# Kernel optimization log

Hardware: AMD Instinct MI355X
Metric: run time of the kernel (lower is better)

Reference implementation:

```python
import jax, jax.numpy as jnp
import numpy as np

B, N, HD = 2, 2048, 2048
NH, KVH = 16, 4
D = HD // NH          # 128
R = NH // KVH         # 4 (kv_ratio)
KVD = KVH * D         # 512


def setup_inputs() -> dict:
    key = jax.random.key(0)
    ks = jax.random.split(key, 6)
    s = 0.02
    return {
        "tokens": jax.random.normal(ks[0], (B, N, HD), jnp.float32),
        "norm_w": jnp.ones((HD,), jnp.float32),
        "Wq": jax.random.normal(ks[1], (HD, HD), jnp.float32) * s,
        "bq": jnp.zeros((HD,), jnp.float32),
        "Wk": jax.random.normal(ks[2], (KVD, HD), jnp.float32) * s,
        "bk": jnp.zeros((KVD,), jnp.float32),
        "Wv": jax.random.normal(ks[3], (KVD, HD), jnp.float32) * s,
        "bv": jnp.zeros((KVD,), jnp.float32),
        "Wo": jax.random.normal(ks[4], (HD, HD), jnp.float32) * s,
        "bo": jnp.zeros((HD,), jnp.float32),
    }


def reference(tokens, norm_w, Wq, bq, Wk, bk, Wv, bv, Wo, bo):
    # RMSNorm (torch default eps=None -> finfo eps), learnable weight
    eps = jnp.finfo(tokens.dtype).eps
    x = tokens * jax.lax.rsqrt(jnp.mean(tokens * tokens, axis=-1, keepdims=True) + eps) * norm_w

    # projections -> [B, heads, N, D]
    q = (x @ Wq.T + bq).reshape(B, N, NH, D).transpose(0, 2, 1, 3)
    k = (x @ Wk.T + bk).reshape(B, N, KVH, D).transpose(0, 2, 1, 3)
    v = (x @ Wv.T + bv).reshape(B, N, KVH, D).transpose(0, 2, 1, 3)

    # GQA via tiling the kv block (matches torch.cat of copies: head h uses kv head h % KVH)
    k = jnp.tile(k, (1, R, 1, 1))
    v = jnp.tile(v, (1, R, 1, 1))

    # Faithful (inverted) mask: True where j <= i, and True positions are masked out.
    mask = jnp.arange(N)[None, :] <= jnp.arange(N)[:, None]  # [N, N]

    # No 1/sqrt(D) scaling in the original
    scores = jnp.einsum('bhid,bhjd->bhij', q, k)
    scores = jnp.where(mask[None, None, :, :], jnp.float32(-1e9), scores)
    attn = jax.nn.softmax(scores, axis=-1)

    a = jnp.einsum('bhij,bhjd->bhid', attn, v)       # [B, NH, N, D]
    a = a.transpose(0, 2, 1, 3).reshape(B, N, HD)    # [B, N, HD]
    return a @ Wo.T + bo
```

## Files before the change

kernel.cpp:

```cpp
#include <hip/hip_runtime.h>

#define BB   2
#define NN   2048
#define HDIM 2048
#define NHD  16
#define KVHD 4
#define DD   128
#define KVW  1024
#define MTOK (BB*NN)

typedef _Float16 h8 __attribute__((ext_vector_type(8)));
typedef _Float16 h4 __attribute__((ext_vector_type(4)));
typedef float    f4 __attribute__((ext_vector_type(4)));
typedef short    b8 __attribute__((ext_vector_type(8)));

static __device__ __forceinline__ f4 mfma16(h8 a, h8 b, f4 c) {
    return __builtin_amdgcn_mfma_f32_16x16x32_f16(a, b, c, 0, 0, 0);
}
static __device__ __forceinline__ f4 mfma16b(b8 a, b8 b, f4 c) {
    return __builtin_amdgcn_mfma_f32_16x16x32_bf16(a, b, c, 0, 0, 0);
}

static __device__ __forceinline__ unsigned short f2bf(float f) {
    unsigned int u = __float_as_uint(f);
    u += 0x7FFF + ((u >> 16) & 1);
    return (unsigned short)(u >> 16);
}

static __device__ __forceinline__ void gload_lds16(const void* g, void* l) {
    __builtin_amdgcn_global_load_lds(
        (const __attribute__((address_space(1))) void*)g,
        (__attribute__((address_space(3))) void*)l, 16, 0, 0);
}

__global__ __launch_bounds__(256) void rmsnorm_k(const float* __restrict__ t,
                                                 const float* __restrict__ wn,
                                                 _Float16* __restrict__ xh) {
    const int row = blockIdx.x, tid = threadIdx.x;
    const float* rp = t + (size_t)row * HDIM;
    float4 v[2];
    float ss = 0.f;
    #pragma unroll
    for (int p = 0; p < 2; ++p) {
        float4 x = *(const float4*)(rp + (p * 256 + tid) * 4);
        v[p] = x;
        ss += x.x * x.x + x.y * x.y + x.z * x.z + x.w * x.w;
    }
    #pragma unroll
    for (int off = 32; off; off >>= 1) ss += __shfl_xor(ss, off, 64);
    __shared__ float sred[4];
    if ((tid & 63) == 0) sred[tid >> 6] = ss;
    __syncthreads();
    float rs = rsqrtf((sred[0] + sred[1] + sred[2] + sred[3]) * (1.0f / HDIM)
                      + 1.1920928955078125e-07f);
    _Float16* op = xh + (size_t)row * HDIM;
    #pragma unroll
    for (int p = 0; p < 2; ++p) {
        int base = (p * 256 + tid) * 4;
        float4 w = *(const float4*)(wn + base);
        h4 o;
        o[0] = (_Float16)(v[p].x * rs * w.x);
        o[1] = (_Float16)(v[p].y * rs * w.y);
        o[2] = (_Float16)(v[p].z * rs * w.z);
        o[3] = (_Float16)(v[p].w * rs * w.w);
        *(h4*)(op + base) = o;
    }
}

__global__ __launch_bounds__(256) void cvt_k(const float* __restrict__ src,
                                             _Float16* __restrict__ dst, int n) {
    int i = (blockIdx.x * 256 + threadIdx.x) * 4;
    if (i < n) {
        float4 v = *(const float4*)(src + i);
        h4 o; o[0] = (_Float16)v.x; o[1] = (_Float16)v.y;
        o[2] = (_Float16)v.z; o[3] = (_Float16)v.w;
        *(h4*)(dst + i) = o;
    }
}

__global__ void biascat_k(const float* __restrict__ bk, const float* __restrict__ bv,
                          float* __restrict__ bkv, float* __restrict__ vsum) {
    int i = blockIdx.x * 256 + threadIdx.x;
    bkv[i] = (i < 512) ? bk[i] : bv[i - 512];
    vsum[i] = 0.f;
}

__global__ __launch_bounds__(256) void vtrans_k(const _Float16* __restrict__ kv,
                                                unsigned short* __restrict__ vt) {
    const int tid = threadIdx.x;
    const int tok = blockIdx.x * 64 + (tid & 63);
    const int kvh = blockIdx.y;
    const int d0 = (tid >> 6) * 32;
    const int b = tok >> 11, n = tok & (NN - 1);
    const _Float16* src = kv + (size_t)tok * KVW + 512 + kvh * DD + d0;
    unsigned short* dstb = vt + ((size_t)(b * KVHD + kvh) * DD) * NN + n;
    #pragma unroll
    for (int u = 0; u < 4; ++u) {
        h8 v = *(const h8*)(src + u * 8);
        #pragma unroll
        for (int e = 0; e < 8; ++e)
            dstb[(size_t)(d0 + u * 8 + e) * NN] = f2bf((float)v[e]);
    }
}

template <int OUTF32>
__global__ __launch_bounds__(256, 2) void gemm_bt(const _Float16* __restrict__ A,
                                                  const _Float16* __restrict__ Bw,
                                                  const float* __restrict__ bias,
                                                  void* __restrict__ Cout,
                                                  int Ndim, int K) {
    __shared__ _Float16 sA[128 * 64];
    __shared__ _Float16 sB[128 * 64];
    const int tid = threadIdx.x;
    const int lane = tid & 63, w = tid >> 6;
    const int ln = lane & 15, quad = lane >> 4;
    const int wm = w >> 1, wn = w & 1;
    const int m0 = blockIdx.y * 128, n0 = blockIdx.x * 128;

    f4 acc[4][4] = {};
    for (int k0 = 0; k0 < K; k0 += 64) {
        #pragma unroll
        for (int it = 0; it < 4; ++it) {
            int chunk = it * 256 + tid;
            int row = chunk >> 3, p = chunk & 7;
            int c = p ^ (row & 7);
            gload_lds16(A + (size_t)(m0 + row) * K + k0 + c * 8, sA + chunk * 8);
            gload_lds16(Bw + (size_t)(n0 + row) * K + k0 + c * 8, sB + chunk * 8);
        }
        __syncthreads();
        #pragma unroll
        for (int kk = 0; kk < 2; ++kk) {
            h8 af[4], bf[4];
            #pragma unroll
            for (int mt = 0; mt < 4; ++mt)
                af[mt] = *(const h8*)&sA[(wm * 64 + mt * 16 + ln) * 64 +
                                         (((kk * 4 + quad) ^ (ln & 7)) << 3)];
            #pragma unroll
            for (int nt = 0; nt < 4; ++nt)
                bf[nt] = *(const h8*)&sB[(wn * 64 + nt * 16 + ln) * 64 +
                                         (((kk * 4 + quad) ^ (ln & 7)) << 3)];
            #pragma unroll
            for (int mt = 0; mt < 4; ++mt)
                #pragma unroll
                for (int nt = 0; nt < 4; ++nt)
                    acc[mt][nt] = mfma16(af[mt], bf[nt], acc[mt][nt]);
        }
        __syncthreads();
    }
    #pragma unroll
    for (int mt = 0; mt < 4; ++mt) {
        int rowb = m0 + wm * 64 + mt * 16 + quad * 4;
        #pragma unroll
        for (int nt = 0; nt < 4; ++nt) {
            int col = n0 + wn * 64 + nt * 16 + ln;
            float bv = bias[col];
            #pragma unroll
            for (int r = 0; r < 4; ++r) {
                float v = acc[mt][nt][r] + bv;
                if (OUTF32)
                    ((float*)Cout)[(size_t)(rowb + r) * Ndim + col] = v;
                else
                    ((_Float16*)Cout)[(size_t)(rowb + r) * Ndim + col] = (_Float16)v;
            }
        }
    }
}

__global__ __launch_bounds__(512, 2) void attn_k(const _Float16* __restrict__ qh,
                                                 const _Float16* __restrict__ kvp,
                                                 const unsigned short* __restrict__ vt,
                                                 _Float16* __restrict__ ah) {
    __shared__ _Float16 s_k[2][32 * 128];
    __shared__ unsigned short s_v[2][128 * 32];
    __shared__ unsigned short s_p[8][32 * 32];
    const int tid = threadIdx.x;
    const int lane = tid & 63, w = tid >> 6;
    const int ln = lane & 15, quad = lane >> 4;
    const int wl = w & 3, half = w >> 2;
    const int u = blockIdx.x;
    const int h = blockIdx.y, b = blockIdx.z;
    const int it0 = half ? (15 - u) : u;
    const int i0 = it0 * 128;
    const int kvh = h & 3;
    const int my_begin = it0 * 4;

    h8 qf[2][4];
    #pragma unroll
    for (int t = 0; t < 2; ++t) {
        const _Float16* qrow =
            qh + ((size_t)(b * NN + i0 + wl * 32 + t * 16 + ln)) * HDIM + h * DD;
        #pragma unroll
        for (int kc = 0; kc < 4; ++kc)
            qf[t][kc] = *(const h8*)(qrow + kc * 32 + quad * 8);
    }

    b8 ones;
    #pragma unroll
    for (int e = 0; e < 8; ++e) ones[e] = (short)0x3F80;

    f4 O[2][8] = {};
    f4 OS[2] = {};

    auto stage = [&](int jt, int bufi) {
        const int j0 = jt * 32;
        {
            int jj = tid >> 4, p = tid & 15;
            int c = p ^ (jj & 15);
            gload_lds16(kvp + ((size_t)(b * NN + j0 + jj)) * KVW + kvh * DD + c * 8,
                        &s_k[bufi][tid * 8]);
        }
        {
            int d = tid >> 2, p = tid & 3;
            int c = p ^ ((d & 3) ^ ((d >> 2) & 3));
            gload_lds16(vt + ((size_t)(b * KVHD + kvh) * DD + d) * NN + j0 + c * 8,
                        &s_v[bufi][tid * 8]);
        }
    };

    const int blk_begin = u * 4;
    stage(blk_begin, 0);
    for (int jt = blk_begin; jt < NN / 32; ++jt) {
        const int j0 = jt * 32;
        const int cur = (jt - blk_begin) & 1;
        __syncthreads();
        if (jt + 1 < NN / 32) stage(jt + 1, cur ^ 1);

        if (jt >= my_begin) {
            f4 sc[2][2] = {};
            #pragma unroll
            for (int nt = 0; nt < 2; ++nt)
                #pragma unroll
                for (int kc = 0; kc < 4; ++kc) {
                    h8 bf = *(const h8*)&s_k[cur][(nt * 16 + ln) * 128 +
                                                  (((kc * 4 + quad) ^ ln) << 3)];
                    sc[0][nt] = mfma16(qf[0][kc], bf, sc[0][nt]);
                    sc[1][nt] = mfma16(qf[1][kc], bf, sc[1][nt]);
                }

            const bool need_mask = (jt < my_begin + 4);
            #pragma unroll
            for (int t = 0; t < 2; ++t) {
                #pragma unroll
                for (int r = 0; r < 4; ++r) {
                    int rr = t * 16 + quad * 4 + r;
                    int sw = r ^ quad;
                    #pragma unroll
                    for (int nt = 0; nt < 2; ++nt) {
                        float s = sc[t][nt][r];
                        if (need_mask) {
                            int ig = i0 + wl * 32 + t * 16 + quad * 4 + r;
                            int jg = j0 + nt * 16 + ln;
                            if (jg <= ig) s = -1e9f;
                        }
                        float p = __expf(s);
                        int c = nt * 2 + (ln >> 3);
                        s_p[w][rr * 32 + ((c ^ sw) << 3) + (ln & 7)] = f2bf(p);
                    }
                }
            }

            const int sv = (ln & 3) ^ ((ln >> 2) & 3);
            #pragma unroll
            for (int t = 0; t < 2; ++t) {
                b8 ap = *(const b8*)&s_p[w][(t * 16 + ln) * 32 + ((quad ^ sv) << 3)];
                #pragma unroll
                for (int dt = 0; dt < 8; ++dt) {
                    b8 bv = *(const b8*)&s_v[cur][(dt * 16 + ln) * 32 +
                                                  ((quad ^ sv) << 3)];
                    O[t][dt] = mfma16b(ap, bv, O[t][dt]);
                }
                OS[t] = mfma16b(ap, ones, OS[t]);
            }
        }
    }

    #pragma unroll
    for (int t = 0; t < 2; ++t) {
        float inv_l[4];
        #pragma unroll
        for (int r = 0; r < 4; ++r) inv_l[r] = 1.0f / OS[t][r];
        #pragma unroll
        for (int dt = 0; dt < 8; ++dt)
            #pragma unroll
            for (int r = 0; r < 4; ++r)
                ah[((size_t)(b * NN + i0 + wl * 32 + t * 16 + quad * 4 + r)) * HDIM +
                   h * DD + dt * 16 + ln] = (_Float16)(O[t][dt][r] * inv_l[r]);
    }
}

__global__ __launch_bounds__(256) void vsum_k(const _Float16* __restrict__ kvp,
                                              float* __restrict__ vsum) {
    __shared__ float red[16][128];
    const int seg = blockIdx.x, kvh = blockIdx.y, b = blockIdx.z;
    const int tid = threadIdx.x;
    const int jj = tid >> 4, dc = (tid & 15) * 8;
    float acc[8] = {};
    #pragma unroll 4
    for (int j = seg * 256 + jj; j < seg * 256 + 256; j += 16) {
        h8 v = *(const h8*)(kvp + ((size_t)(b * NN + j)) * KVW + 512 + kvh * DD + dc);
        #pragma unroll
        for (int e = 0; e < 8; ++e) acc[e] += (float)v[e];
    }
    #pragma unroll
    for (int e = 0; e < 8; ++e) red[jj][dc + e] = acc[e];
    __syncthreads();
    if (tid < 128) {
        float s = 0.f;
        #pragma unroll
        for (int t = 0; t < 16; ++t) s += red[t][tid];
        atomicAdd(&vsum[(b * KVHD + kvh) * DD + tid], s);
    }
}

__global__ void fixup_write_k(const float* __restrict__ vsum,
                              _Float16* __restrict__ ah) {
    int b = blockIdx.x >> 2, kvh = blockIdx.x & 3, d = threadIdx.x;
    float mean = vsum[(b * KVHD + kvh) * DD + d] * (1.0f / NN);
    #pragma unroll
    for (int r = 0; r < 4; ++r) {
        int h = r * 4 + kvh;
        ah[((size_t)(b * NN + NN - 1)) * HDIM + h * DD + d] = (_Float16)mean;
    }
}

extern "C" void kernel_launch(void* const* d_in, const int* in_sizes, int n_in,
                              void* d_out, int out_size, void* d_ws, size_t ws_size,
                              hipStream_t stream) {
    const float* tokens = (const float*)d_in[0];
    const float* norm_w = (const float*)d_in[1];
    const float* Wq = (const float*)d_in[2];
    const float* bq = (const float*)d_in[3];
    const float* Wk = (const float*)d_in[4];
    const float* bk = (const float*)d_in[5];
    const float* Wv = (const float*)d_in[6];
    const float* bv = (const float*)d_in[7];
    const float* Wo = (const float*)d_in[8];
    const float* bo = (const float*)d_in[9];
    float* out = (float*)d_out;

    char* ws = (char*)d_ws;
    _Float16* x_h   = (_Float16*)(ws);
    _Float16* wq_h  = (_Float16*)(ws + 16777216);
    _Float16* wkv_h = (_Float16*)(ws + 25165824);
    _Float16* wo_h  = (_Float16*)(ws + 29360128);
    float*    bkv   = (float*)   (ws + 37748736);
    _Float16* q_h   = (_Float16*)(ws + 37752832);
    _Float16* kv_h  = (_Float16*)(ws + 54530048);
    _Float16* a_h   = (_Float16*)(ws + 62918656);
    unsigned short* vt_h = (unsigned short*)(ws + 79695872);
    float*    vsum  = (float*)   (ws + 81793024);

    rmsnorm_k<<<MTOK, 256, 0, stream>>>(tokens, norm_w, x_h);
    cvt_k<<<4096, 256, 0, stream>>>(Wq, wq_h, HDIM * HDIM);
    cvt_k<<<1024, 256, 0, stream>>>(Wk, wkv_h, 512 * HDIM);
    cvt_k<<<1024, 256, 0, stream>>>(Wv, wkv_h + 512 * HDIM, 512 * HDIM);
    cvt_k<<<4096, 256, 0, stream>>>(Wo, wo_h, HDIM * HDIM);
    biascat_k<<<4, 256, 0, stream>>>(bk, bv, bkv, vsum);

    gemm_bt<0><<<dim3(HDIM / 128, MTOK / 128), 256, 0, stream>>>(
        x_h, wq_h, bq, (void*)q_h, HDIM, HDIM);
    gemm_bt<0><<<dim3(KVW / 128, MTOK / 128), 256, 0, stream>>>(
        x_h, wkv_h, bkv, (void*)kv_h, KVW, HDIM);

    vtrans_k<<<dim3(MTOK / 64, KVHD), 256, 0, stream>>>(kv_h, vt_h);

    attn_k<<<dim3(8, NHD, BB), 512, 0, stream>>>(q_h, kv_h, vt_h, a_h);
    vsum_k<<<dim3(8, KVHD, BB), 256, 0, stream>>>(kv_h, vsum);
    fixup_write_k<<<BB * KVHD, 128, 0, stream>>>(vsum, a_h);

    gemm_bt<1><<<dim3(HDIM / 128, MTOK / 128), 256, 0, stream>>>(
        a_h, wo_h, bo, (void*)out, HDIM, HDIM);
}
```

Measured before the change: 340.7 us.

## Restructure attention to 32x32 bf16 MFMA for PV with 64-key tiles

Switches the P·V product from 16x16x32 to 32x32x16 bf16 MFMA and computes scores transposed (K as A operand) so each lane packs four probabilities into one 8-byte LDS store. Key/value tiles grow from 32 to 64 keys. Blocks shrink from 512 to 256 threads with one query tile per block, and load balancing now pairs tiles across the batch instead of within a block. This is meant to cut MFMA issue count and LDS traffic per key, at the cost of more LDS per block and different occupancy.

```diff
diff --git a/kernel.cpp b/kernel.cpp
--- a/kernel.cpp
+++ b/kernel.cpp
@@ -12,13 +12,14 @@
 typedef _Float16 h8 __attribute__((ext_vector_type(8)));
 typedef _Float16 h4 __attribute__((ext_vector_type(4)));
 typedef float    f4 __attribute__((ext_vector_type(4)));
+typedef float    fx16 __attribute__((ext_vector_type(16)));
 typedef short    b8 __attribute__((ext_vector_type(8)));
 
 static __device__ __forceinline__ f4 mfma16(h8 a, h8 b, f4 c) {
     return __builtin_amdgcn_mfma_f32_16x16x32_f16(a, b, c, 0, 0, 0);
 }
-static __device__ __forceinline__ f4 mfma16b(b8 a, b8 b, f4 c) {
-    return __builtin_amdgcn_mfma_f32_16x16x32_bf16(a, b, c, 0, 0, 0);
+static __device__ __forceinline__ fx16 mfma32b(b8 a, b8 b, fx16 c) {
+    return __builtin_amdgcn_mfma_f32_32x32x16_bf16(a, b, c, 0, 0, 0);
 }
 
 static __device__ __forceinline__ unsigned short f2bf(float f) {
@@ -166,29 +167,27 @@
     }
 }
 
-__global__ __launch_bounds__(512, 2) void attn_k(const _Float16* __restrict__ qh,
+__global__ __launch_bounds__(256, 2) void attn_k(const _Float16* __restrict__ qh,
                                                  const _Float16* __restrict__ kvp,
                                                  const unsigned short* __restrict__ vt,
                                                  _Float16* __restrict__ ah) {
-    __shared__ _Float16 s_k[2][32 * 128];
-    __shared__ unsigned short s_v[2][128 * 32];
-    __shared__ unsigned short s_p[8][32 * 32];
+    __shared__ _Float16 s_k[2][64 * 128];
+    __shared__ unsigned short s_v[2][128 * 64];
+    __shared__ unsigned short s_p[4][32 * 32];
     const int tid = threadIdx.x;
     const int lane = tid & 63, w = tid >> 6;
     const int ln = lane & 15, quad = lane >> 4;
-    const int wl = w & 3, half = w >> 2;
-    const int u = blockIdx.x;
+    const int l5 = lane & 31, hi = lane >> 5;
     const int h = blockIdx.y, b = blockIdx.z;
-    const int it0 = half ? (15 - u) : u;
+    const int it0 = b ? (15 - (int)blockIdx.x) : (int)blockIdx.x;
     const int i0 = it0 * 128;
     const int kvh = h & 3;
-    const int my_begin = it0 * 4;
 
     h8 qf[2][4];
     #pragma unroll
     for (int t = 0; t < 2; ++t) {
         const _Float16* qrow =
-            qh + ((size_t)(b * NN + i0 + wl * 32 + t * 16 + ln)) * HDIM + h * DD;
+            qh + ((size_t)(b * NN + i0 + w * 32 + t * 16 + ln)) * HDIM + h * DD;
         #pragma unroll
         for (int kc = 0; kc < 4; ++kc)
             qf[t][kc] = *(const h8*)(qrow + kc * 32 + quad * 8);
@@ -198,94 +197,100 @@
     #pragma unroll
     for (int e = 0; e < 8; ++e) ones[e] = (short)0x3F80;
 
-    f4 O[2][8] = {};
-    f4 OS[2] = {};
+    fx16 O[4] = {};
+    fx16 OS = {};
 
     auto stage = [&](int jt, int bufi) {
-        const int j0 = jt * 32;
-        {
-            int jj = tid >> 4, p = tid & 15;
+        const int j0s = jt * 64;
+        #pragma unroll
+        for (int itr = 0; itr < 4; ++itr) {
+            int chunk = itr * 256 + tid;
+            int jj = chunk >> 4, p = chunk & 15;
             int c = p ^ (jj & 15);
-            gload_lds16(kvp + ((size_t)(b * NN + j0 + jj)) * KVW + kvh * DD + c * 8,
-                        &s_k[bufi][tid * 8]);
-        }
-        {
-            int d = tid >> 2, p = tid & 3;
-            int c = p ^ ((d & 3) ^ ((d >> 2) & 3));
-            gload_lds16(vt + ((size_t)(b * KVHD + kvh) * DD + d) * NN + j0 + c * 8,
-                        &s_v[bufi][tid * 8]);
+            gload_lds16(kvp + ((size_t)(b * NN + j0s + jj)) * KVW + kvh * DD + c * 8,
+                        &s_k[bufi][chunk * 8]);
+        }
+        #pragma unroll
+        for (int itr = 0; itr < 4; ++itr) {
+            int chunk = itr * 256 + tid;
+            int d = chunk >> 3, p = chunk & 7;
+            int c = p ^ (d & 7);
+            gload_lds16(vt + ((size_t)(b * KVHD + kvh) * DD + d) * NN + j0s + c * 8,
+                        &s_v[bufi][chunk * 8]);
         }
     };
 
-    const int blk_begin = u * 4;
-    stage(blk_begin, 0);
-    for (int jt = blk_begin; jt < NN / 32; ++jt) {
-        const int j0 = jt * 32;
-        const int cur = (jt - blk_begin) & 1;
+    const int jt0 = it0 * 2;
+    stage(jt0, 0);
+    for (int jt = jt0; jt < 32; ++jt) {
+        const int j0 = jt * 64;
+        const int cur = (jt - jt0) & 1;
         __syncthreads();
-        if (jt + 1 < NN / 32) stage(jt + 1, cur ^ 1);
-
-        if (jt >= my_begin) {
-            f4 sc[2][2] = {};
-            #pragma unroll
-            for (int nt = 0; nt < 2; ++nt)
+        if (jt + 1 < 32) stage(jt + 1, cur ^ 1);
+
+        f4 sc[2][4] = {};
+        #pragma unroll
+        for (int nt = 0; nt < 4; ++nt)
+            #pragma unroll
+            for (int kc = 0; kc < 4; ++kc) {
+                h8 kf = *(const h8*)&s_k[cur][(nt * 16 + ln) * 128 +
+                                              (((kc * 4 + quad) ^ ln) << 3)];
+                sc[0][nt] = mfma16(kf, qf[0][kc], sc[0][nt]);
+                sc[1][nt] = mfma16(kf, qf[1][kc], sc[1][nt]);
+            }
+
+        const bool need_mask = (jt < jt0 + 2);
+        #pragma unroll
+        for (int half = 0; half < 2; ++half) {
+            #pragma unroll
+            for (int t = 0; t < 2; ++t)
                 #pragma unroll
-                for (int kc = 0; kc < 4; ++kc) {
-                    h8 bf = *(const h8*)&s_k[cur][(nt * 16 + ln) * 128 +
-                                                  (((kc * 4 + quad) ^ ln) << 3)];
-                    sc[0][nt] = mfma16(qf[0][kc], bf, sc[0][nt]);
-                    sc[1][nt] = mfma16(qf[1][kc], bf, sc[1][nt]);
-                }
-
-            const bool need_mask = (jt < my_begin + 4);
-            #pragma unroll
-            for (int t = 0; t < 2; ++t) {
-                #pragma unroll
-                for (int r = 0; r < 4; ++r) {
-                    int rr = t * 16 + quad * 4 + r;
-                    int sw = r ^ quad;
+                for (int nn = 0; nn < 2; ++nn) {
+                    int nt = half * 2 + nn;
+                    float pv[4];
                     #pragma unroll
-                    for (int nt = 0; nt < 2; ++nt) {
+                    for (int r = 0; r < 4; ++r) {
                         float s = sc[t][nt][r];
                         if (need_mask) {
-                            int ig = i0 + wl * 32 + t * 16 + quad * 4 + r;
-                            int jg = j0 + nt * 16 + ln;
+                            int ig = i0 + w * 32 + t * 16 + ln;
+                            int jg = j0 + nt * 16 + quad * 4 + r;
                             if (jg <= ig) s = -1e9f;
                         }
-                        float p = __expf(s);
-                        int c = nt * 2 + (ln >> 3);
-                        s_p[w][rr * 32 + ((c ^ sw) << 3) + (ln & 7)] = f2bf(p);
+                        pv[r] = __expf(s);
                     }
+                    unsigned int u0 = f2bf(pv[0]) | ((unsigned int)f2bf(pv[1]) << 16);
+                    unsigned int u1 = f2bf(pv[2]) | ((unsigned int)f2bf(pv[3]) << 16);
+                    int addr = (t * 16 + ln) * 32 +
+                               (((nn * 2 + (quad >> 1)) ^ (ln & 3)) << 3) +
+                               ((quad & 1) << 2);
+                    *(uint2*)&s_p[w][addr] = make_uint2(u0, u1);
                 }
+            #pragma unroll
+            for (int ks = 0; ks < 2; ++ks) {
+                b8 ap = *(const b8*)&s_p[w][l5 * 32 +
+                                            (((ks * 2 + hi) ^ (l5 & 3)) << 3)];
+                #pragma unroll
+                for (int nt4 = 0; nt4 < 4; ++nt4) {
+                    b8 bv = *(const b8*)&s_v[cur][(nt4 * 32 + l5) * 64 +
+                                                  (((half * 4 + ks * 2 + hi) ^ (l5 & 7)) << 3)];
+                    O[nt4] = mfma32b(ap, bv, O[nt4]);
+                }
+                OS = mfma32b(ap, ones, OS);
             }
-
-            const int sv = (ln & 3) ^ ((ln >> 2) & 3);
-            #pragma unroll
-            for (int t = 0; t < 2; ++t) {
-                b8 ap = *(const b8*)&s_p[w][(t * 16 + ln) * 32 + ((quad ^ sv) << 3)];
-                #pragma unroll
-                for (int dt = 0; dt < 8; ++dt) {
-                    b8 bv = *(const b8*)&s_v[cur][(dt * 16 + ln) * 32 +
-                                                  ((quad ^ sv) << 3)];
-                    O[t][dt] = mfma16b(ap, bv, O[t][dt]);
-                }
-                OS[t] = mfma16b(ap, ones, OS[t]);
-            }
-        }
-    }
-
-    #pragma unroll
-    for (int t = 0; t < 2; ++t) {
-        float inv_l[4];
-        #pragma unroll
-        for (int r = 0; r < 4; ++r) inv_l[r] = 1.0f / OS[t][r];
-        #pragma unroll
-        for (int dt = 0; dt < 8; ++dt)
-            #pragma unroll
-            for (int r = 0; r < 4; ++r)
-                ah[((size_t)(b * NN + i0 + wl * 32 + t * 16 + quad * 4 + r)) * HDIM +
-                   h * DD + dt * 16 + ln] = (_Float16)(O[t][dt][r] * inv_l[r]);
-    }
+        }
+    }
+
+    float inv_l[16];
+    #pragma unroll
+    for (int rg = 0; rg < 16; ++rg) inv_l[rg] = 1.0f / OS[rg];
+    #pragma unroll
+    for (int nt4 = 0; nt4 < 4; ++nt4)
+        #pragma unroll
+        for (int rg = 0; rg < 16; ++rg) {
+            int q = (rg & 3) + 8 * (rg >> 2) + 4 * hi;
+            ah[((size_t)(b * NN + i0 + w * 32 + q)) * HDIM + h * DD + nt4 * 32 + l5] =
+                (_Float16)(O[nt4][rg] * inv_l[rg]);
+        }
 }
 
 __global__ __launch_bounds__(256) void vsum_k(const _Float16* __restrict__ kvp,
@@ -364,7 +369,7 @@
 
     vtrans_k<<<dim3(MTOK / 64, KVHD), 256, 0, stream>>>(kv_h, vt_h);
 
-    attn_k<<<dim3(8, NHD, BB), 512, 0, stream>>>(q_h, kv_h, vt_h, a_h);
+    attn_k<<<dim3(16, NHD, BB), 256, 0, stream>>>(q_h, kv_h, vt_h, a_h);
     vsum_k<<<dim3(8, KVHD, BB), 256, 0, stream>>>(kv_h, vsum);
     fixup_write_k<<<BB * KVHD, 128, 0, stream>>>(vsum, a_h);
 
```

Result: faster. 327.3 us (-3.9%).
